# Performance work log

Hardware: AMD Instinct MI355X
Metric: run time of the kernel (lower is better)

Reference implementation:

```python
import jax, jax.numpy as jnp
import numpy as np

NQ, NL, QD, LD, H = 100000, 32, 384, 1024, 128
E, E_SEE, E_PRED = 1000000, 750000, 250000
N = NQ + NL
EPS = 1e-5


def _bn(x, g, b):
    # BatchNorm1d in training mode: biased batch statistics over node dim
    mu = x.mean(0)
    var = x.var(0)
    return g * (x - mu) * jax.lax.rsqrt(var + EPS) + b


def _general_conv(x, src, dst, ea, Wm, bm, We, be_):
    # PyG GeneralConv (heads=1, no attention, aggr='add', in==out -> identity skip)
    msg = x[src] @ Wm + bm + ea @ We + be_            # [E_see, H]
    agg = jax.ops.segment_sum(msg, dst, num_segments=N)
    return agg + x


def setup_inputs() -> dict:
    key = jax.random.key(0)
    ks = jax.random.split(key, 20)
    s = lambda fan_in: 1.0 / np.sqrt(fan_in)
    return {
        'query_features': jax.random.normal(ks[0], (NQ, QD), jnp.float32),
        'llm_features': jax.random.normal(ks[1], (NL, LD), jnp.float32),
        'edge_index': jax.random.randint(ks[2], (2, E), 0, N, jnp.int64 if jax.config.jax_enable_x64 else jnp.int32),
        'edge_mask': jax.random.randint(ks[3], (E_PRED,), 0, E),
        'edge_can_see': jax.random.randint(ks[4], (E_SEE,), 0, E),
        'edge_weight': jax.random.uniform(ks[5], (E, 1), jnp.float32),
        'Wq': jax.random.normal(ks[6], (QD, H), jnp.float32) * s(QD),
        'bq': jnp.zeros((H,), jnp.float32),
        'Wl': jax.random.normal(ks[7], (LD, H), jnp.float32) * s(LD),
        'bl': jnp.zeros((H,), jnp.float32),
        'W_em': jax.random.normal(ks[8], (1, 1), jnp.float32),
        'b_em': jnp.zeros((1,), jnp.float32),
        'W1m': jax.random.normal(ks[9], (H, H), jnp.float32) * s(H),
        'b1m': jnp.zeros((H,), jnp.float32),
        'W1e': jax.random.normal(ks[10], (1, H), jnp.float32),
        'b1e': jnp.zeros((H,), jnp.float32),
        'W2m': jax.random.normal(ks[11], (H, H), jnp.float32) * s(H),
        'b2m': jnp.zeros((H,), jnp.float32),
        'W2e': jax.random.normal(ks[12], (1, H), jnp.float32),
        'b2e': jnp.zeros((H,), jnp.float32),
        'g1': jnp.ones((H,), jnp.float32), 'beta1': jnp.zeros((H,), jnp.float32),
        'g2': jnp.ones((H,), jnp.float32), 'beta2': jnp.zeros((H,), jnp.float32),
    }


def reference(query_features, llm_features, edge_index, edge_mask, edge_can_see,
              edge_weight, Wq, bq, Wl, bl, W_em, b_em, W1m, b1m, W1e, b1e,
              W2m, b2m, W2e, b2e, g1, beta1, g2, beta2):
    lrelu = jax.nn.leaky_relu  # slope 0.01 (torch default)
    ei_mask = edge_index[:, edge_can_see]       # [2, E_see]
    ei_pred = edge_index[:, edge_mask]          # [2, E_pred]
    ew = lrelu(edge_weight[edge_can_see] @ W_em + b_em)  # [E_see, 1]
    # feature alignment
    x_ini = jnp.concatenate([query_features @ Wq + bq, llm_features @ Wl + bl], 0)  # [N, H]
    src, dst = ei_mask[0], ei_mask[1]
    x = lrelu(_bn(_general_conv(x_ini, src, dst, ew, W1m, b1m, W1e, b1e), g1, beta1))
    x = _bn(_general_conv(x, src, dst, ew, W2m, b2m, W2e, b2e), g2, beta2)
    edge_predict = jax.nn.sigmoid((x_ini[ei_pred[0]] * x[ei_pred[1]]).mean(-1))  # [E_pred]
    return edge_predict
```

## Files before the change

kernel.cpp:

```cpp
#include <hip/hip_runtime.h>
#include <math.h>

#define NQ 100000
#define NL 32
#define QD 384
#define LD 1024
#define H 128
#define E_TOT 1000000
#define E_SEE 750000
#define E_PRED 250000
#define NN (NQ + NL)
#define EPS 1e-5f

#define NB_SCAN ((NN + 255) / 256)
#define NB_GEMM ((NN + 127) / 128)
#define NB_XINI ((NQ + 127) / 128)

typedef __attribute__((ext_vector_type(8))) short short8;
typedef __attribute__((ext_vector_type(4))) short short4v;
typedef __attribute__((ext_vector_type(4))) float f32x4;
typedef __attribute__((ext_vector_type(4))) unsigned int uint4v;

__device__ __forceinline__ unsigned short f2bf(float f) {
  unsigned int u = __builtin_bit_cast(unsigned int, f);
  u = (u + 0x7FFFu + ((u >> 16) & 1u)) >> 16;
  return (unsigned short)u;
}


__global__ void k_ew_hist(const int* __restrict__ ecs, const int* __restrict__ EI,
                          const float* __restrict__ ewt, const float* __restrict__ Wem,
                          const float* __restrict__ bem, float* __restrict__ ew,
                          int* __restrict__ cnt) {
  int e = blockIdx.x * 256 + threadIdx.x;
  if (e >= E_SEE) return;
  int idx = ecs[e];
  int d = EI[E_TOT + idx];
  atomicAdd(&cnt[d], 1);
  float w = ewt[idx] * Wem[0] + bem[0];
  ew[e] = w > 0.f ? w : 0.01f * w;
}

__global__ void k_scan_block(const int* __restrict__ cnt, int* __restrict__ bsum) {
  __shared__ int red[256];
  int i = blockIdx.x * 256 + threadIdx.x;
  red[threadIdx.x] = (i < NN) ? cnt[i] : 0;
  __syncthreads();
  for (int s = 128; s > 0; s >>= 1) {
    if (threadIdx.x < s) red[threadIdx.x] += red[threadIdx.x + s];
    __syncthreads();
  }
  if (threadIdx.x == 0) bsum[blockIdx.x] = red[0];
}

__global__ void k_scan_top(const int* __restrict__ bsum, int* __restrict__ boff) {
  __shared__ int buf[2][512];
  int t = threadIdx.x;
  int v = (t < NB_SCAN) ? bsum[t] : 0;
  buf[0][t] = v;
  __syncthreads();
  int src = 0;
  for (int d = 1; d < 512; d <<= 1) {
    int x = buf[src][t];
    if (t >= d) x += buf[src][t - d];
    buf[src ^ 1][t] = x;
    __syncthreads();
    src ^= 1;
  }
  if (t < NB_SCAN) boff[t] = buf[src][t] - v;
}

__global__ void k_scan_write(const int* __restrict__ cnt, const int* __restrict__ boff,
                             int* __restrict__ off) {
  __shared__ int buf[2][256];
  int t = threadIdx.x;
  int i = blockIdx.x * 256 + t;
  int v = (i < NN) ? cnt[i] : 0;
  buf[0][t] = v;
  __syncthreads();
  int src = 0;
  for (int d = 1; d < 256; d <<= 1) {
    int x = buf[src][t];
    if (t >= d) x += buf[src][t - d];
    buf[src ^ 1][t] = x;
    __syncthreads();
    src ^= 1;
  }
  if (i < NN) off[i] = boff[blockIdx.x] + buf[src][t] - v;
  if (i == 0) off[NN] = E_SEE;
}

__global__ void k_fill(const int* __restrict__ ecs, const int* __restrict__ EI,
                       const float* __restrict__ ew, const int* __restrict__ off,
                       int* __restrict__ cur, int* __restrict__ csr_src,
                       float* __restrict__ csr_ew) {
  int e = blockIdx.x * 256 + threadIdx.x;
  if (e >= E_SEE) return;
  int idx = ecs[e];
  int s = EI[idx];
  int d = EI[E_TOT + idx];
  int p = off[d] + atomicAdd(&cur[d], 1);
  csr_src[p] = s;
  csr_ew[p] = ew[e];
}


__global__ void k_prep(const float* __restrict__ Wq, const float* __restrict__ W1m,
                       const float* __restrict__ W2m,
                       unsigned short* __restrict__ Wqt, unsigned short* __restrict__ W1t,
                       unsigned short* __restrict__ W2t) {
  int i = blockIdx.x * 256 + threadIdx.x;
  const int tot1 = QD * H;
  const int tot2 = H * H;
  if (i < tot1) {
    int n = i / QD, k = i - n * QD;
    Wqt[i] = f2bf(Wq[(size_t)k * H + n]);
  } else if (i < tot1 + tot2) {
    int j = i - tot1;
    int n = j >> 7, k = j & 127;
    W1t[j] = f2bf(W1m[(size_t)k * H + n]);
  } else if (i < tot1 + 2 * tot2) {
    int j = i - tot1 - tot2;
    int n = j >> 7, k = j & 127;
    W2t[j] = f2bf(W2m[(size_t)k * H + n]);
  }
}


__global__ __launch_bounds__(128) void k_llm_part(const float* __restrict__ lf,
                                                  const float* __restrict__ Wl,
                                                  float* __restrict__ part) {
  int r = blockIdx.x >> 3;
  int s = blockIdx.x & 7;
  int t = threadIdx.x;
  int k0 = s * 128;
  float acc = 0.f;
#pragma unroll 4
  for (int k = 0; k < 128; k += 4) {
    float a0 = lf[(size_t)r * LD + k0 + k + 0];
    float a1 = lf[(size_t)r * LD + k0 + k + 1];
    float a2 = lf[(size_t)r * LD + k0 + k + 2];
    float a3 = lf[(size_t)r * LD + k0 + k + 3];
    acc = fmaf(a0, Wl[(size_t)(k0 + k + 0) * H + t], acc);
    acc = fmaf(a1, Wl[(size_t)(k0 + k + 1) * H + t], acc);
    acc = fmaf(a2, Wl[(size_t)(k0 + k + 2) * H + t], acc);
    acc = fmaf(a3, Wl[(size_t)(k0 + k + 3) * H + t], acc);
  }
  part[(size_t)blockIdx.x * 128 + t] = acc;
}

__global__ void k_llm_comb(const float* __restrict__ part, const float* __restrict__ bl,
                           float* __restrict__ XINI) {
  int i = blockIdx.x * 256 + threadIdx.x;
  if (i >= NL * H) return;
  int r = i >> 7, t = i & 127;
  float a = bl[t];
#pragma unroll
  for (int s = 0; s < 8; s++) a += part[(size_t)(r * 8 + s) * 128 + t];
  XINI[(size_t)(NQ + r) * H + t] = a;
}


__global__ __launch_bounds__(256, 3) void k_xini(
    const float* __restrict__ qf, const unsigned short* __restrict__ Wqt,
    const float* __restrict__ bq, float* __restrict__ XINI) {
  int tid = threadIdx.x;
  int lane = tid & 63;
  int w = tid >> 6;
  int l15 = lane & 15, quad = lane >> 4;
  int rowbase = blockIdx.x * 128 + w * 32;

  f32x4 acc[2][8];
#pragma unroll
  for (int i = 0; i < 2; ++i)
#pragma unroll
    for (int j = 0; j < 8; ++j) acc[i][j] = (f32x4){0.f, 0.f, 0.f, 0.f};

  int r0 = rowbase + l15;
  int r1 = rowbase + 16 + l15;
  const float* rp0 = qf + (size_t)r0 * QD + quad * 8;
  const float* rp1 = qf + (size_t)r1 * QD + quad * 8;
  bool v0 = r0 < NQ, v1 = r1 < NQ;
  const unsigned short* bp = Wqt + (size_t)l15 * QD + quad * 8;

  const float4 z4 = make_float4(0.f, 0.f, 0.f, 0.f);
  float4 pfa[2][2][2];
#pragma unroll
  for (int s = 0; s < 2; ++s) {
    int ko = s * 32;
    pfa[s][0][0] = v0 ? *(const float4*)(rp0 + ko) : z4;
    pfa[s][0][1] = v0 ? *(const float4*)(rp0 + ko + 4) : z4;
    pfa[s][1][0] = v1 ? *(const float4*)(rp1 + ko) : z4;
    pfa[s][1][1] = v1 ? *(const float4*)(rp1 + ko + 4) : z4;
  }

#define XSTEP(KB, SLOT)                                                        \
  do {                                                                         \
    short8 bfr[8];                                                             \
    _Pragma("unroll")                                                          \
    for (int nt = 0; nt < 8; ++nt)                                             \
      bfr[nt] = *(const short8*)(bp + (size_t)nt * 16 * QD + (KB));            \
    short8 af[2];                                                              \
    _Pragma("unroll")                                                          \
    for (int mt = 0; mt < 2; ++mt) {                                           \
      uint4v pk;                                                               \
      pk.x = ((unsigned int)f2bf(pfa[SLOT][mt][0].y) << 16) |                  \
             f2bf(pfa[SLOT][mt][0].x);                                         \
      pk.y = ((unsigned int)f2bf(pfa[SLOT][mt][0].w) << 16) |                  \
             f2bf(pfa[SLOT][mt][0].z);                                         \
      pk.z = ((unsigned int)f2bf(pfa[SLOT][mt][1].y) << 16) |                  \
             f2bf(pfa[SLOT][mt][1].x);                                         \
      pk.w = ((unsigned int)f2bf(pfa[SLOT][mt][1].w) << 16) |                  \
             f2bf(pfa[SLOT][mt][1].z);                                         \
      af[mt] = __builtin_bit_cast(short8, pk);                                 \
    }                                                                          \
    if ((KB) + 64 < 384) {                   \
      int ko = (KB) + 64;                                                      \
      pfa[SLOT][0][0] = v0 ? *(const float4*)(rp0 + ko) : z4;                  \
      pfa[SLOT][0][1] = v0 ? *(const float4*)(rp0 + ko + 4) : z4;              \
      pfa[SLOT][1][0] = v1 ? *(const float4*)(rp1 + ko) : z4;                  \
      pfa[SLOT][1][1] = v1 ? *(const float4*)(rp1 + ko + 4) : z4;              \
    }                                                                          \
    _Pragma("unroll")                                                          \
    for (int mt = 0; mt < 2; ++mt)                                             \
      _Pragma("unroll")                                                        \
      for (int nt = 0; nt < 8; ++nt)                                           \
        acc[mt][nt] = __builtin_amdgcn_mfma_f32_16x16x32_bf16(                 \
            af[mt], bfr[nt], acc[mt][nt], 0, 0, 0);                            \
  } while (0)

  for (int kb = 0; kb < 384; kb += 64) {
    XSTEP(kb, 0);
    XSTEP(kb + 32, 1);
  }
#undef XSTEP

  float bias[8];
#pragma unroll
  for (int nt = 0; nt < 8; ++nt) bias[nt] = bq[nt * 16 + l15];
#pragma unroll
  for (int mt = 0; mt < 2; ++mt) {
#pragma unroll
    for (int r = 0; r < 4; ++r) {
      int n = rowbase + mt * 16 + quad * 4 + r;
      if (n < NQ) {
#pragma unroll
        for (int nt = 0; nt < 8; ++nt)
          XINI[(size_t)n * H + nt * 16 + l15] = acc[mt][nt][r] + bias[nt];
      }
    }
  }
}


template <bool TRANS>
__global__ __launch_bounds__(256) void k_seg(
    const float* __restrict__ Xin, const int* __restrict__ off,
    const int* __restrict__ csr_src, const float* __restrict__ csr_ew,
    const float* __restrict__ scale, const float* __restrict__ shift,
    unsigned short* __restrict__ S16, float* __restrict__ swsum,
    float* __restrict__ degf) {
  int w = blockIdx.x * 4 + (threadIdx.x >> 6);
  if (w >= NN) return;
  int lane = threadIdx.x & 63;
  int o0 = off[w], o1 = off[w + 1];
  float ax = 1.f, ay = 1.f, bx = 0.f, by = 0.f;
  if (TRANS) {
    float2 sc = *(const float2*)&scale[lane * 2];
    float2 sh = *(const float2*)&shift[lane * 2];
    ax = sc.x; ay = sc.y; bx = sh.x; by = sh.y;
  }
  float accx = 0.f, accy = 0.f, ews = 0.f;
  for (int k = o0; k < o1; ++k) {
    int s = csr_src[k];
    float2 v = *(const float2*)&Xin[(size_t)s * H + lane * 2];
    if (TRANS) {
      float t0 = fmaf(ax, v.x, bx); v.x = t0 > 0.f ? t0 : 0.01f * t0;
      float t1 = fmaf(ay, v.y, by); v.y = t1 > 0.f ? t1 : 0.01f * t1;
    }
    accx += v.x; accy += v.y;
    ews += csr_ew[k];
  }
  unsigned int pk = ((unsigned int)f2bf(accy) << 16) | f2bf(accx);
  *(unsigned int*)&S16[(size_t)w * H + lane * 2] = pk;
  if (lane == 0) { swsum[w] = ews; degf[w] = (float)(o1 - o0); }
}


template <bool TRANS>
__global__ __launch_bounds__(256) void k_gemm(
    const unsigned short* __restrict__ S16, const float* __restrict__ Xin,
    float* __restrict__ Xout, const unsigned short* __restrict__ Wt,
    const float* __restrict__ bm, const float* __restrict__ be,
    const float* __restrict__ We,
    const float* __restrict__ scale, const float* __restrict__ shift,
    const float* __restrict__ swsum, const float* __restrict__ degf,
    float* __restrict__ partials) {
  __shared__ unsigned short sA[128][40];
  __shared__ unsigned short sB[128][40];
  __shared__ float st[2][8][128];
  int tid = threadIdx.x;
  int w = tid >> 6, lane = tid & 63;
  int l15 = lane & 15, quad = lane >> 4;
  int wr = (w >> 1) * 64, wc = (w & 1) * 64;
  int rowbase = blockIdx.x * 128;
  f32x4 acc[4][4];
#pragma unroll
  for (int i = 0; i < 4; i++)
#pragma unroll
    for (int j = 0; j < 4; j++) acc[i][j] = (f32x4){0.f, 0.f, 0.f, 0.f};

  int arow = tid >> 1, ah = (tid & 1) * 16;
  int4 pa[2], pb[2];
  {
    int gr = rowbase + arow;
    if (gr < NN) {
      pa[0] = *(const int4*)&S16[(size_t)gr * H + ah];
      pa[1] = *(const int4*)&S16[(size_t)gr * H + ah + 8];
    } else {
      pa[0] = make_int4(0, 0, 0, 0); pa[1] = make_int4(0, 0, 0, 0);
    }
    pb[0] = *(const int4*)&Wt[(size_t)arow * H + ah];
    pb[1] = *(const int4*)&Wt[(size_t)arow * H + ah + 8];
  }
  for (int step = 0; step < 4; ++step) {
    *(int4*)&sA[arow][ah] = pa[0];
    *(int4*)&sA[arow][ah + 8] = pa[1];
    *(int4*)&sB[arow][ah] = pb[0];
    *(int4*)&sB[arow][ah + 8] = pb[1];
    __syncthreads();
    if (step + 1 < 4) {
      int kn = (step + 1) * 32;
      int gr = rowbase + arow;
      if (gr < NN) {
        pa[0] = *(const int4*)&S16[(size_t)gr * H + kn + ah];
        pa[1] = *(const int4*)&S16[(size_t)gr * H + kn + ah + 8];
      } else {
        pa[0] = make_int4(0, 0, 0, 0); pa[1] = make_int4(0, 0, 0, 0);
      }
      pb[0] = *(const int4*)&Wt[(size_t)arow * H + kn + ah];
      pb[1] = *(const int4*)&Wt[(size_t)arow * H + kn + ah + 8];
    }
    short8 af[4], bfr[4];
#pragma unroll
    for (int mt = 0; mt < 4; ++mt)
      af[mt] = *(const short8*)&sA[wr + mt * 16 + l15][quad * 8];
#pragma unroll
    for (int nt = 0; nt < 4; ++nt)
      bfr[nt] = *(const short8*)&sB[wc + nt * 16 + l15][quad * 8];
#pragma unroll
    for (int mt = 0; mt < 4; ++mt)
#pragma unroll
      for (int nt = 0; nt < 4; ++nt)
        acc[mt][nt] = __builtin_amdgcn_mfma_f32_16x16x32_bf16(
            af[mt], bfr[nt], acc[mt][nt], 0, 0, 0);
    __syncthreads();
  }
  int col4[4];
  float cb4[4], we4[4], sc4[4], sh4[4], ps[4], pq[4];
#pragma unroll
  for (int nt = 0; nt < 4; ++nt) {
    int col = wc + nt * 16 + l15;
    col4[nt] = col;
    cb4[nt] = bm[col] + be[col];
    we4[nt] = We[col];
    if (TRANS) { sc4[nt] = scale[col]; sh4[nt] = shift[col]; }
    ps[nt] = 0.f; pq[nt] = 0.f;
  }
#pragma unroll
  for (int mt = 0; mt < 4; ++mt) {
#pragma unroll
    for (int r = 0; r < 4; ++r) {
      int n = rowbase + wr + mt * 16 + quad * 4 + r;
      if (n < NN) {
        float dg = degf[n], sw = swsum[n];
#pragma unroll
        for (int nt = 0; nt < 4; ++nt) {
          float rr = Xin[(size_t)n * H + col4[nt]];
          if (TRANS) {
            float t = fmaf(sc4[nt], rr, sh4[nt]);
            rr = t > 0.f ? t : 0.01f * t;
          }
          float o = acc[mt][nt][r] + dg * cb4[nt] + sw * we4[nt] + rr;
          Xout[(size_t)n * H + col4[nt]] = o;
          ps[nt] += o; pq[nt] += o * o;
        }
      }
    }
  }
  int slot = (w >> 1) * 4 + quad;
#pragma unroll
  for (int nt = 0; nt < 4; ++nt) {
    st[0][slot][col4[nt]] = ps[nt];
    st[1][slot][col4[nt]] = pq[nt];
  }
  __syncthreads();
  int plane = tid >> 7, col = tid & 127;
  float s = 0.f;
#pragma unroll
  for (int y = 0; y < 8; y++) s += st[plane][y][col];
  partials[(size_t)blockIdx.x * 256 + tid] = s;
}


__global__ __launch_bounds__(256) void k_bnstats(
    const float* __restrict__ partials, const float* __restrict__ g,
    const float* __restrict__ beta, float* __restrict__ scale,
    float* __restrict__ shift) {
  __shared__ float rs[256], rq[256];
  int j = blockIdx.x;
  int t = threadIdx.x;
  float as = 0.f, aq = 0.f;
  for (int b = t; b < NB_GEMM; b += 256) {
    as += partials[(size_t)b * 256 + j];
    aq += partials[(size_t)b * 256 + 128 + j];
  }
  rs[t] = as; rq[t] = aq;
  __syncthreads();
  for (int s = 128; s > 0; s >>= 1) {
    if (t < s) { rs[t] += rs[t + s]; rq[t] += rq[t + s]; }
    __syncthreads();
  }
  if (t == 0) {
    float mean = rs[0] / (float)NN;
    float var = rq[0] / (float)NN - mean * mean;
    float a = g[j] * rsqrtf(var + EPS);
    scale[j] = a;
    shift[j] = beta[j] - mean * a;
  }
}


__global__ __launch_bounds__(256) void k_pred(
    const int* __restrict__ emask, const int* __restrict__ EI,
    const float* __restrict__ XINI, const float* __restrict__ X,
    const float* __restrict__ scale, const float* __restrict__ shift,
    float* __restrict__ out) {
  int i = blockIdx.x * 4 + (threadIdx.x >> 6);
  if (i >= E_PRED) return;
  int lane = threadIdx.x & 63;
  int m = emask[i];
  int p0 = EI[m];
  int p1 = EI[E_TOT + m];
  float2 a = *(const float2*)&XINI[(size_t)p0 * H + lane * 2];
  float2 b = *(const float2*)&X[(size_t)p1 * H + lane * 2];
  float2 sc = *(const float2*)&scale[lane * 2];
  float2 sh = *(const float2*)&shift[lane * 2];
  float v = a.x * fmaf(sc.x, b.x, sh.x) + a.y * fmaf(sc.y, b.y, sh.y);
#pragma unroll
  for (int mm = 32; mm > 0; mm >>= 1) v += __shfl_xor(v, mm, 64);
  if (lane == 0) out[i] = 1.f / (1.f + expf(-v * (1.f / 128.f)));
}


extern "C" void kernel_launch(void* const* d_in, const int* in_sizes, int n_in,
                              void* d_out, int out_size, void* d_ws, size_t ws_size,
                              hipStream_t stream) {
  const float* qf    = (const float*)d_in[0];
  const float* lf    = (const float*)d_in[1];
  const int*   EI    = (const int*)d_in[2];
  const int*   emask = (const int*)d_in[3];
  const int*   ecs   = (const int*)d_in[4];
  const float* ewt   = (const float*)d_in[5];
  const float* Wq    = (const float*)d_in[6];
  const float* bq    = (const float*)d_in[7];
  const float* Wl    = (const float*)d_in[8];
  const float* bl    = (const float*)d_in[9];
  const float* Wem   = (const float*)d_in[10];
  const float* bem   = (const float*)d_in[11];
  const float* W1m   = (const float*)d_in[12];
  const float* b1m   = (const float*)d_in[13];
  const float* W1e   = (const float*)d_in[14];
  const float* b1e   = (const float*)d_in[15];
  const float* W2m   = (const float*)d_in[16];
  const float* b2m   = (const float*)d_in[17];
  const float* W2e   = (const float*)d_in[18];
  const float* b2e   = (const float*)d_in[19];
  const float* g1    = (const float*)d_in[20];
  const float* beta1 = (const float*)d_in[21];
  const float* g2    = (const float*)d_in[22];
  const float* beta2 = (const float*)d_in[23];
  float* out = (float*)d_out;

  char* p = (char*)d_ws;
  auto alloc = [&](size_t bytes) -> void* {
    void* r = (void*)p;
    p += (bytes + 255) & ~(size_t)255;
    return r;
  };
  float* XINI    = (float*)alloc((size_t)NN * H * 4);
  float* X       = (float*)alloc((size_t)NN * H * 4);
  unsigned short* S16 = (unsigned short*)alloc((size_t)NN * H * 2);
  float* ew      = (float*)alloc((size_t)E_SEE * 4);
  float* csr_ew  = (float*)alloc((size_t)E_SEE * 4);
  int*   csr_src = (int*)alloc((size_t)E_SEE * 4);
  int*   cnt     = (int*)alloc((size_t)NN * 4);
  int*   off     = (int*)alloc((size_t)(NN + 1) * 4);
  int*   cur     = (int*)alloc((size_t)NN * 4);
  int*   bsum    = (int*)alloc((size_t)NB_SCAN * 4);
  int*   boff    = (int*)alloc((size_t)NB_SCAN * 4);
  float* swsum   = (float*)alloc((size_t)NN * 4);
  float* degf    = (float*)alloc((size_t)NN * 4);
  float* partials= (float*)alloc((size_t)NB_GEMM * 256 * 4);
  float* scale1  = (float*)alloc(128 * 4);
  float* shift1  = (float*)alloc(128 * 4);
  float* scale2  = (float*)alloc(128 * 4);
  float* shift2  = (float*)alloc(128 * 4);
  unsigned short* Wqt = (unsigned short*)alloc((size_t)QD * H * 2);
  unsigned short* W1t = (unsigned short*)alloc((size_t)H * H * 2);
  unsigned short* W2t = (unsigned short*)alloc((size_t)H * H * 2);
  float* llmpart = (float*)alloc((size_t)NL * 8 * H * 4);

  hipMemsetAsync(cnt, 0, (size_t)NN * 4, stream);
  hipMemsetAsync(cur, 0, (size_t)NN * 4, stream);

  int ebl = (E_SEE + 255) / 256;
  k_prep<<<320, 256, 0, stream>>>(Wq, W1m, W2m, Wqt, W1t, W2t);
  k_ew_hist<<<ebl, 256, 0, stream>>>(ecs, EI, ewt, Wem, bem, ew, cnt);
  k_scan_block<<<NB_SCAN, 256, 0, stream>>>(cnt, bsum);
  k_scan_top<<<1, 512, 0, stream>>>(bsum, boff);
  k_scan_write<<<NB_SCAN, 256, 0, stream>>>(cnt, boff, off);
  k_fill<<<ebl, 256, 0, stream>>>(ecs, EI, ew, off, cur, csr_src, csr_ew);

  k_llm_part<<<NL * 8, 128, 0, stream>>>(lf, Wl, llmpart);
  k_llm_comb<<<(NL * H + 255) / 256, 256, 0, stream>>>(llmpart, bl, XINI);
  k_xini<<<NB_XINI, 256, 0, stream>>>(qf, Wqt, bq, XINI);

  int segbl = (NN + 3) / 4;
  k_seg<false><<<segbl, 256, 0, stream>>>(XINI, off, csr_src, csr_ew,
                                          nullptr, nullptr, S16, swsum, degf);
  k_gemm<false><<<NB_GEMM, 256, 0, stream>>>(S16, XINI, X, W1t, b1m, b1e, W1e,
                                             nullptr, nullptr, swsum, degf, partials);
  k_bnstats<<<H, 256, 0, stream>>>(partials, g1, beta1, scale1, shift1);
  k_seg<true><<<segbl, 256, 0, stream>>>(X, off, csr_src, csr_ew,
                                         scale1, shift1, S16, swsum, degf);
  k_gemm<true><<<NB_GEMM, 256, 0, stream>>>(S16, X, X, W2t, b2m, b2e, W2e,
                                            scale1, shift1, swsum, degf, partials);
  k_bnstats<<<H, 256, 0, stream>>>(partials, g2, beta2, scale2, shift2);
  int pbl = (E_PRED + 3) / 4;
  k_pred<<<pbl, 256, 0, stream>>>(emask, EI, XINI, X, scale2, shift2, out);
}
```

Measured before the change: 781.6 us.

## Stage Wq tile in double-buffered LDS for k_xini MFMA GEMM

Instead of each wave loading its bf16 Wq fragments straight from global memory, the block cooperatively loads each 128x32 slice of the transposed weight into a double-buffered shared-memory tile. Waves then read their B fragments from LDS, with the next slice prefetched into registers and written into the other buffer after the MFMAs. This cuts redundant global/L2 traffic for the weight across the four waves. In exchange it adds a __syncthreads per k-step and some LDS pressure, which may affect occupancy.

```diff
diff --git a/kernel.cpp b/kernel.cpp
--- a/kernel.cpp
+++ b/kernel.cpp
@@ -164,12 +164,17 @@
 __global__ __launch_bounds__(256, 3) void k_xini(
     const float* __restrict__ qf, const unsigned short* __restrict__ Wqt,
     const float* __restrict__ bq, float* __restrict__ XINI) {
+  __shared__ unsigned short sB[2][128][40];
   int tid = threadIdx.x;
   int lane = tid & 63;
   int w = tid >> 6;
   int l15 = lane & 15, quad = lane >> 4;
   int rowbase = blockIdx.x * 128 + w * 32;
 
+  int trow = tid >> 1;
+  int tk = (tid & 1) * 16;
+  const unsigned short* bgp = Wqt + (size_t)trow * QD + tk;
+
   f32x4 acc[2][8];
 #pragma unroll
   for (int i = 0; i < 2; ++i)
@@ -181,57 +186,70 @@
   const float* rp0 = qf + (size_t)r0 * QD + quad * 8;
   const float* rp1 = qf + (size_t)r1 * QD + quad * 8;
   bool v0 = r0 < NQ, v1 = r1 < NQ;
-  const unsigned short* bp = Wqt + (size_t)l15 * QD + quad * 8;
-
   const float4 z4 = make_float4(0.f, 0.f, 0.f, 0.f);
-  float4 pfa[2][2][2];
-#pragma unroll
-  for (int s = 0; s < 2; ++s) {
-    int ko = s * 32;
-    pfa[s][0][0] = v0 ? *(const float4*)(rp0 + ko) : z4;
-    pfa[s][0][1] = v0 ? *(const float4*)(rp0 + ko + 4) : z4;
-    pfa[s][1][0] = v1 ? *(const float4*)(rp1 + ko) : z4;
-    pfa[s][1][1] = v1 ? *(const float4*)(rp1 + ko + 4) : z4;
-  }
-
-#define XSTEP(KB, SLOT)                                                        \
+
+  {
+    int4 g0 = *(const int4*)(bgp + 0);
+    int4 g1 = *(const int4*)(bgp + 8);
+    *(int4*)&sB[0][trow][tk] = g0;
+    *(int4*)&sB[0][trow][tk + 8] = g1;
+  }
+  float4 s0a = v0 ? *(const float4*)(rp0 + 0) : z4;
+  float4 s0b = v0 ? *(const float4*)(rp0 + 4) : z4;
+  float4 s0c = v1 ? *(const float4*)(rp1 + 0) : z4;
+  float4 s0d = v1 ? *(const float4*)(rp1 + 4) : z4;
+  float4 s1a = v0 ? *(const float4*)(rp0 + 32) : z4;
+  float4 s1b = v0 ? *(const float4*)(rp0 + 36) : z4;
+  float4 s1c = v1 ? *(const float4*)(rp1 + 32) : z4;
+  float4 s1d = v1 ? *(const float4*)(rp1 + 36) : z4;
+  __syncthreads();
+
+#define XSTEP(KB, BUF, RA0, RA1, RB0, RB1)                                     \
   do {                                                                         \
+    int4 g0, g1;                                                               \
+    bool stage = (KB) + 32 < 384;                                              \
+    if (stage) {                     \
+      g0 = *(const int4*)(bgp + (KB) + 32);                                    \
+      g1 = *(const int4*)(bgp + (KB) + 40);                                    \
+    }                                                                          \
     short8 bfr[8];                                                             \
     _Pragma("unroll")                                                          \
     for (int nt = 0; nt < 8; ++nt)                                             \
-      bfr[nt] = *(const short8*)(bp + (size_t)nt * 16 * QD + (KB));            \
-    short8 af[2];                                                              \
-    _Pragma("unroll")                                                          \
-    for (int mt = 0; mt < 2; ++mt) {                                           \
-      uint4v pk;                                                               \
-      pk.x = ((unsigned int)f2bf(pfa[SLOT][mt][0].y) << 16) |                  \
-             f2bf(pfa[SLOT][mt][0].x);                                         \
-      pk.y = ((unsigned int)f2bf(pfa[SLOT][mt][0].w) << 16) |                  \
-             f2bf(pfa[SLOT][mt][0].z);                                         \
-      pk.z = ((unsigned int)f2bf(pfa[SLOT][mt][1].y) << 16) |                  \
-             f2bf(pfa[SLOT][mt][1].x);                                         \
-      pk.w = ((unsigned int)f2bf(pfa[SLOT][mt][1].w) << 16) |                  \
-             f2bf(pfa[SLOT][mt][1].z);                                         \
-      af[mt] = __builtin_bit_cast(short8, pk);                                 \
-    }                                                                          \
-    if ((KB) + 64 < 384) {                   \
-      int ko = (KB) + 64;                                                      \
-      pfa[SLOT][0][0] = v0 ? *(const float4*)(rp0 + ko) : z4;                  \
-      pfa[SLOT][0][1] = v0 ? *(const float4*)(rp0 + ko + 4) : z4;              \
-      pfa[SLOT][1][0] = v1 ? *(const float4*)(rp1 + ko) : z4;                  \
-      pfa[SLOT][1][1] = v1 ? *(const float4*)(rp1 + ko + 4) : z4;              \
+      bfr[nt] = *(const short8*)&sB[BUF][nt * 16 + l15][quad * 8];             \
+    uint4v pk0, pk1;                                                           \
+    pk0.x = ((unsigned int)f2bf(RA0.y) << 16) | f2bf(RA0.x);                   \
+    pk0.y = ((unsigned int)f2bf(RA0.w) << 16) | f2bf(RA0.z);                   \
+    pk0.z = ((unsigned int)f2bf(RA1.y) << 16) | f2bf(RA1.x);                   \
+    pk0.w = ((unsigned int)f2bf(RA1.w) << 16) | f2bf(RA1.z);                   \
+    pk1.x = ((unsigned int)f2bf(RB0.y) << 16) | f2bf(RB0.x);                   \
+    pk1.y = ((unsigned int)f2bf(RB0.w) << 16) | f2bf(RB0.z);                   \
+    pk1.z = ((unsigned int)f2bf(RB1.y) << 16) | f2bf(RB1.x);                   \
+    pk1.w = ((unsigned int)f2bf(RB1.w) << 16) | f2bf(RB1.z);                   \
+    short8 af0 = __builtin_bit_cast(short8, pk0);                              \
+    short8 af1 = __builtin_bit_cast(short8, pk1);                              \
+    if ((KB) + 64 < 384) {                 \
+      RA0 = v0 ? *(const float4*)(rp0 + (KB) + 64) : z4;                       \
+      RA1 = v0 ? *(const float4*)(rp0 + (KB) + 68) : z4;                       \
+      RB0 = v1 ? *(const float4*)(rp1 + (KB) + 64) : z4;                       \
+      RB1 = v1 ? *(const float4*)(rp1 + (KB) + 68) : z4;                       \
     }                                                                          \
     _Pragma("unroll")                                                          \
-    for (int mt = 0; mt < 2; ++mt)                                             \
-      _Pragma("unroll")                                                        \
-      for (int nt = 0; nt < 8; ++nt)                                           \
-        acc[mt][nt] = __builtin_amdgcn_mfma_f32_16x16x32_bf16(                 \
-            af[mt], bfr[nt], acc[mt][nt], 0, 0, 0);                            \
+    for (int nt = 0; nt < 8; ++nt) {                                           \
+      acc[0][nt] = __builtin_amdgcn_mfma_f32_16x16x32_bf16(af0, bfr[nt],       \
+                                                           acc[0][nt], 0, 0, 0); \
+      acc[1][nt] = __builtin_amdgcn_mfma_f32_16x16x32_bf16(af1, bfr[nt],       \
+                                                           acc[1][nt], 0, 0, 0); \
+    }                                                                          \
+    if (stage) {         \
+      *(int4*)&sB[(BUF) ^ 1][trow][tk] = g0;                                   \
+      *(int4*)&sB[(BUF) ^ 1][trow][tk + 8] = g1;                               \
+      __syncthreads();                                                         \
+    }                                                                          \
   } while (0)
 
   for (int kb = 0; kb < 384; kb += 64) {
-    XSTEP(kb, 0);
-    XSTEP(kb + 32, 1);
+    XSTEP(kb, 0, s0a, s0b, s0c, s0d);
+    XSTEP(kb + 32, 1, s1a, s1b, s1c, s1d);
   }
 #undef XSTEP
 
```

New measurement: 770.9 us. About the same (-1.4%).
